# Performance work log

Measured on AMD Instinct MI355X. Metric: run time of the kernel, lower is better.

Reference implementation:

```python
import jax, jax.numpy as jnp
import numpy as np

B, S, D = 1, 2048, 2048
H = 16
Q_LORA = 1536
KV_LORA = 512
NOPE = 128
ROPE = 64
VD = 128
QHD = NOPE + ROPE  # 192
THETA = 50000.0
EPS = 1e-6


def rmsnorm(x, w, eps=EPS):
    xf = x.astype(jnp.float32)
    var = jnp.mean(xf * xf, axis=-1, keepdims=True)
    return (w * (xf * jax.lax.rsqrt(var + eps)).astype(x.dtype))


def rotate_half(x):
    x1, x2 = jnp.split(x, 2, axis=-1)
    return jnp.concatenate([-x2, x1], axis=-1)


def deinterleave(x):
    # view(..., d//2, 2).transpose(-1,-2).reshape(..., d): [x0,x2,...,x1,x3,...]
    b, h, s, d = x.shape
    return x.reshape(b, h, s, d // 2, 2).swapaxes(-1, -2).reshape(b, h, s, d)


def setup_inputs() -> dict:
    key = jax.random.key(0)
    ks = jax.random.split(key, 8)
    sc = 0.02
    return {
        "hidden_states": jax.random.normal(ks[0], (B, S, D), jnp.float32),
        "position_ids": jnp.broadcast_to(jnp.arange(S, dtype=jnp.int32), (B, S)),
        "q_a_w": jax.random.normal(ks[1], (Q_LORA, D), jnp.float32) * sc,
        "q_a_ln_w": jnp.ones((Q_LORA,), jnp.float32),
        "q_b_w": jax.random.normal(ks[2], (H * QHD, Q_LORA), jnp.float32) * sc,
        "kv_a_w": jax.random.normal(ks[3], (KV_LORA + ROPE, D), jnp.float32) * sc,
        "kv_a_ln_w": jnp.ones((KV_LORA,), jnp.float32),
        "kv_b_w": jax.random.normal(ks[4], (H * (NOPE + VD), KV_LORA), jnp.float32) * sc,
        "o_w": jax.random.normal(ks[5], (D, H * VD), jnp.float32) * sc,
    }


def reference(hidden_states, position_ids, q_a_w, q_a_ln_w, q_b_w, kv_a_w, kv_a_ln_w, kv_b_w, o_w):
    bsz, q_len, _ = hidden_states.shape
    # low-rank Q: q_b(rmsnorm(q_a(x)))
    q = rmsnorm(hidden_states @ q_a_w.T, q_a_ln_w) @ q_b_w.T
    q = q.reshape(bsz, q_len, H, QHD).transpose(0, 2, 1, 3)  # [b,h,s,192]
    q_nope, q_pe = q[..., :NOPE], q[..., NOPE:]
    # compressed KV + shared rope key
    ckv = hidden_states @ kv_a_w.T  # [b,s,512+64]
    compressed_kv, k_pe = ckv[..., :KV_LORA], ckv[..., KV_LORA:]
    k_pe = k_pe.reshape(bsz, q_len, 1, ROPE).transpose(0, 2, 1, 3)  # [b,1,s,64]
    kv = rmsnorm(compressed_kv, kv_a_ln_w) @ kv_b_w.T
    kv = kv.reshape(bsz, q_len, H, NOPE + VD).transpose(0, 2, 1, 3)
    k_nope, value_states = kv[..., :NOPE], kv[..., NOPE:]
    # rotary cache
    inv_freq = 1.0 / (THETA ** (jnp.arange(0, ROPE, 2, dtype=jnp.float32) / ROPE))
    t = jnp.arange(q_len, dtype=jnp.float32)
    freqs = jnp.outer(t, inv_freq)
    emb = jnp.concatenate([freqs, freqs], axis=-1)  # [s,64]
    cos = jnp.cos(emb)[position_ids][:, None]  # [b,1,s,64]
    sin = jnp.sin(emb)[position_ids][:, None]
    q_pe = deinterleave(q_pe)
    k_pe = deinterleave(k_pe)
    q_pe = q_pe * cos + rotate_half(q_pe) * sin
    k_pe = k_pe * cos + rotate_half(k_pe) * sin
    query_states = jnp.concatenate([q_nope, q_pe], axis=-1)  # [b,h,s,192]
    key_states = jnp.concatenate([k_nope, jnp.broadcast_to(k_pe, (bsz, H, q_len, ROPE))], axis=-1)
    scale = QHD ** (-0.5)
    scores = jnp.einsum('bhqd,bhkd->bhqk', query_states, key_states) * scale
    causal = jnp.tril(jnp.ones((q_len, q_len), bool))
    scores = jnp.where(causal, scores, jnp.finfo(scores.dtype).min)
    attn = jax.nn.softmax(scores, axis=-1)
    out = jnp.einsum('bhqk,bhkd->bhqd', attn, value_states)  # [b,h,s,128]
    out = out.transpose(0, 2, 1, 3).reshape(bsz, q_len, H * VD)
    return out @ o_w.T
```

## Files before the change

### kernel.cpp

```cpp
#include <hip/hip_runtime.h>
#include <hip/hip_bf16.h>
#include <cmath>

#define S_LEN 2048
#define D_MODEL 2048
#define N_HEADS 16
#define Q_LORA 1536
#define KV_LORA 512
#define NOPE 128
#define ROPE_D 64
#define VD 128
#define QHD 192
#define AC_W 2112

typedef __attribute__((ext_vector_type(8))) short bf16x8;
typedef __attribute__((ext_vector_type(4))) float f32x4;
typedef __attribute__((ext_vector_type(4))) unsigned short u16x4;

static __device__ __forceinline__ unsigned short f2u(float x) {
  union { float f; unsigned u; } v; v.f = x;
  unsigned r = v.u + 0x7fffu + ((v.u >> 16) & 1u);
  return (unsigned short)(r >> 16);
}
static __device__ __forceinline__ unsigned short f2u_fast(float x) {
  union { float f; unsigned u; } v; v.f = x;
  return (unsigned short)((v.u + 0x8000u) >> 16);
}
static __device__ __forceinline__ float u2f(unsigned short x) {
  union { unsigned u; float f; } v; v.u = ((unsigned)x) << 16;
  return v.f;
}

#define AS1 __attribute__((address_space(1)))
#define AS3 __attribute__((address_space(3)))
static __device__ __forceinline__ void gload_lds16(const unsigned short* g, unsigned short* l) {
  __builtin_amdgcn_global_load_lds((const AS1 unsigned int*)g, (AS3 unsigned int*)l, 16, 0, 0);
}

__global__ __launch_bounds__(256) void conv_bf16(const float* __restrict__ src,
                                                 unsigned short* __restrict__ dst,
                                                 int n4, float scale) {
  for (int i = blockIdx.x * 256 + threadIdx.x; i < n4; i += gridDim.x * 256) {
    const float4 v = ((const float4*)src)[i];
    u16x4 o;
    o[0] = f2u(v.x * scale); o[1] = f2u(v.y * scale);
    o[2] = f2u(v.z * scale); o[3] = f2u(v.w * scale);
    ((u16x4*)dst)[i] = o;
  }
}

__global__ __launch_bounds__(256) void conv2_bf16(const float* __restrict__ srcA, int n4a,
                                                  const float* __restrict__ srcB, int n4total,
                                                  unsigned short* __restrict__ dst) {
  for (int i = blockIdx.x * 256 + threadIdx.x; i < n4total; i += gridDim.x * 256) {
    const float4 v = (i < n4a) ? ((const float4*)srcA)[i] : ((const float4*)srcB)[i - n4a];
    u16x4 o;
    o[0] = f2u(v.x); o[1] = f2u(v.y); o[2] = f2u(v.z); o[3] = f2u(v.w);
    ((u16x4*)dst)[i] = o;
  }
}

template <int MODE>
__global__ __launch_bounds__(256) void gemm_mfma(const unsigned short* __restrict__ A,
                                                 const unsigned short* __restrict__ W,
                                                 void* __restrict__ Cv,
                                                 unsigned short* __restrict__ C2,
                                                 int N, int K) {
  __shared__ unsigned short As[2][8192];
  __shared__ unsigned short Ws[2][4096];
  const int tid = threadIdx.x;
  const int wave = tid >> 6, lane = tid & 63;
  const int col16 = lane & 15, g = lane >> 4;
  const int arow = blockIdx.y * 128, wrow = blockIdx.x * 64;
  const int wm = (wave >> 1) * 64, wn = (wave & 1) * 32;

  const unsigned short* gA[4];
  const unsigned short* gW[2];
  int dA[4], dW[2];
#pragma unroll
  for (int i = 0; i < 4; ++i) {
    const int c = i * 256 + tid;
    const int r = c >> 3, sl = c & 7;
    gA[i] = A + (size_t)(arow + r) * K + (sl ^ (r & 7)) * 8;
    dA[i] = c * 8;
  }
#pragma unroll
  for (int i = 0; i < 2; ++i) {
    const int c = i * 256 + tid;
    const int r = c >> 3, sl = c & 7;
    gW[i] = W + (size_t)(wrow + r) * K + (sl ^ (r & 7)) * 8;
    dW[i] = c * 8;
  }

  f32x4 acc[4][2];
#pragma unroll
  for (int i = 0; i < 4; ++i)
#pragma unroll
    for (int j = 0; j < 2; ++j) acc[i][j] = (f32x4){0.f, 0.f, 0.f, 0.f};

#pragma unroll
  for (int i = 0; i < 4; ++i) gload_lds16(gA[i], &As[0][dA[i]]);
#pragma unroll
  for (int i = 0; i < 2; ++i) gload_lds16(gW[i], &Ws[0][dW[i]]);

  int cur = 0;
  for (int k0 = 0; k0 < K; k0 += 64) {
    __syncthreads();
    if (k0 + 64 < K) {
      const int b = cur ^ 1, kk = k0 + 64;
#pragma unroll
      for (int i = 0; i < 4; ++i) gload_lds16(gA[i] + kk, &As[b][dA[i]]);
#pragma unroll
      for (int i = 0; i < 2; ++i) gload_lds16(gW[i] + kk, &Ws[b][dW[i]]);
    }
#pragma unroll
    for (int kh = 0; kh < 2; ++kh) {
      bf16x8 af[4], bfr[2];
#pragma unroll
      for (int i = 0; i < 4; ++i) {
        const int row = wm + i * 16 + col16;
        af[i] = *(const bf16x8*)(&As[cur][row * 64 + (((kh * 4 + g) ^ (row & 7)) * 8)]);
      }
#pragma unroll
      for (int j = 0; j < 2; ++j) {
        const int row = wn + j * 16 + col16;
        bfr[j] = *(const bf16x8*)(&Ws[cur][row * 64 + (((kh * 4 + g) ^ (row & 7)) * 8)]);
      }
#pragma unroll
      for (int i = 0; i < 4; ++i)
#pragma unroll
        for (int j = 0; j < 2; ++j)
          acc[i][j] = __builtin_amdgcn_mfma_f32_16x16x32_bf16(af[i], bfr[j], acc[i][j], 0, 0, 0);
    }
    cur ^= 1;
  }

#pragma unroll
  for (int i = 0; i < 4; ++i)
#pragma unroll
    for (int j = 0; j < 2; ++j) {
      const int col = wrow + wn + j * 16 + col16;
      const int row0 = arow + wm + i * 16 + g * 4;
#pragma unroll
      for (int r = 0; r < 4; ++r) {
        if constexpr (MODE == 0)
          ((float*)Cv)[(size_t)(row0 + r) * N + col] = acc[i][j][r];
        else if constexpr (MODE == 1)
          ((unsigned short*)Cv)[(size_t)(row0 + r) * N + col] = f2u(acc[i][j][r]);
        else {
          const int hh = col >> 8, d = col & 255;
          if (d < NOPE)
            C2[((size_t)hh * S_LEN + row0 + r) * QHD + d] = f2u(acc[i][j][r]);
          else
            ((unsigned short*)Cv)[(size_t)(row0 + r) * (N_HEADS * 256) + col] = f2u(acc[i][j][r]);
        }
      }
    }
}

__global__ __launch_bounds__(256) void rmsnorm2_kernel(const float* __restrict__ ac,
                                                       const float* __restrict__ wq,
                                                       const float* __restrict__ wkv,
                                                       unsigned short* __restrict__ qan,
                                                       unsigned short* __restrict__ ckvn) {
  const int row = blockIdx.x;
  const bool kv = blockIdx.y != 0;
  const float* x = ac + (size_t)row * AC_W + (kv ? Q_LORA : 0);
  const float* w = kv ? wkv : wq;
  unsigned short* dst = kv ? (ckvn + (size_t)row * KV_LORA) : (qan + (size_t)row * Q_LORA);
  const int dim = kv ? KV_LORA : Q_LORA;
  float ss = 0.f;
  for (int i = threadIdx.x; i < dim; i += 256) {
    float v = x[i];
    ss += v * v;
  }
#pragma unroll
  for (int off = 32; off; off >>= 1) ss += __shfl_xor(ss, off);
  __shared__ float red[4];
  const int wv = threadIdx.x >> 6, ln = threadIdx.x & 63;
  if (ln == 0) red[wv] = ss;
  __syncthreads();
  const float tot = red[0] + red[1] + red[2] + red[3];
  const float scale = rsqrtf(tot / (float)dim + 1e-6f);
  for (int i = threadIdx.x; i < dim; i += 256) {
    dst[i] = f2u(w[i] * (x[i] * scale));
  }
}

__global__ void rope_kernel(unsigned short* __restrict__ q, const float* __restrict__ ac,
                            unsigned short* __restrict__ Kb, const int* __restrict__ pos_ids) {
  const int s = blockIdx.x;
  const int j = threadIdx.x;
  const float t = (float)pos_ids[s];
  const float invf = powf(50000.0f, -(float)(2 * j) / 64.0f);
  const float ang = t * invf;
  const float c = cosf(ang), sn = sinf(ang);
  for (int h = 0; h < N_HEADS; ++h) {
    unsigned short* base = q + (size_t)s * (N_HEADS * QHD) + h * QHD + NOPE;
    const float x0 = u2f(base[2 * j]), x1 = u2f(base[2 * j + 1]);
    __syncthreads();
    base[j] = f2u(x0 * c - x1 * sn);
    base[32 + j] = f2u(x1 * c + x0 * sn);
    __syncthreads();
  }
  const float* kb = ac + (size_t)s * AC_W + 2048;
  const unsigned short r0 = f2u(kb[2 * j] * c - kb[2 * j + 1] * sn);
  const unsigned short r1 = f2u(kb[2 * j + 1] * c + kb[2 * j] * sn);
#pragma unroll
  for (int h = 0; h < N_HEADS; ++h) {
    unsigned short* kd = Kb + ((size_t)h * S_LEN + s) * QHD + NOPE;
    kd[j] = r0;
    kd[32 + j] = r1;
  }
}

__global__ __launch_bounds__(256) void build_vt(const unsigned short* __restrict__ kv,
                                                unsigned short* __restrict__ Vt) {
  __shared__ unsigned short t[32][33];
  const int s0 = blockIdx.x * 32, d0 = blockIdx.y * 32, h = blockIdx.z;
  const int tx = threadIdx.x & 31, ty = threadIdx.x >> 5;
#pragma unroll
  for (int i = 0; i < 4; ++i) {
    const int s = s0 + ty + i * 8;
    t[ty + i * 8][tx] = kv[(size_t)s * (N_HEADS * 256) + h * 256 + NOPE + d0 + tx];
  }
  __syncthreads();
  const int p = ((tx & 15) >> 2) * 8 + ((tx >> 4) & 1) * 4 + (tx & 3);
#pragma unroll
  for (int i = 0; i < 4; ++i) {
    const int d = d0 + ty + i * 8;
    Vt[((size_t)h * VD + d) * S_LEN + s0 + p] = t[tx][ty + i * 8];
  }
}

__global__ __launch_bounds__(256, 4) void flash_attn(const unsigned short* __restrict__ Q,
                                                     const unsigned short* __restrict__ Kb,
                                                     const unsigned short* __restrict__ Vt,
                                                     unsigned short* __restrict__ Pb,
                                                     float2* __restrict__ mlb) {
  __shared__ unsigned short Ks[2][32 * QHD];
  __shared__ unsigned short Vs[2][VD * 32];
  const int tid = threadIdx.x;
  const int wave = tid >> 6, lane = tid & 63;
  const int g = lane >> 4, col = lane & 15;
  const int lin = (int)blockIdx.x;
  const int h = ((lin & 7) << 1) | ((lin >> 3) & 1);
  const int s = (lin >> 4) & 1;
  const int z = lin >> 5;
  int t;
  if (z < 8) t = 31 - z;
  else if (z < 16) t = z - 8;
  else if (z < 24) t = 39 - z;
  else t = z - 16;
  const int qw = t * 64 + wave * 16;
  const int qr = qw + col;

  bf16x8 qf[6];
  {
    const unsigned short* qrow = Q + (size_t)qr * (N_HEADS * QHD) + h * QHD + g * 8;
#pragma unroll
    for (int i = 0; i < 6; ++i) qf[i] = *(const bf16x8*)(qrow + i * 32);
  }

  const unsigned short* KbH = Kb + (size_t)h * S_LEN * QHD;
  const unsigned short* VtH = Vt + (size_t)h * VD * S_LEN;

  int eK[3], eV[2];
#pragma unroll
  for (int i = 0; i < 3; ++i) {
    const int c = i * 256 + tid;
    const int r = c / 24, sl = c - r * 24;
    eK[i] = r * QHD + (((sl & 24) | ((sl & 7) ^ (r & 7)))) * 8;
  }
#pragma unroll
  for (int i = 0; i < 2; ++i) {
    const int c = i * 256 + tid;
    const int d = c >> 2, sl = c & 3;
    eV[i] = d * S_LEN + ((sl ^ (d & 3))) * 8;
  }

  f32x4 o[8];
#pragma unroll
  for (int i = 0; i < 8; ++i) o[i] = (f32x4){0.f, 0.f, 0.f, 0.f};
  float m = -1e30f, l = 0.f;

  const int nT = t + 1;

  {
    const unsigned short* kp = KbH + (size_t)s * 32 * QHD;
    const unsigned short* vp = VtH + s * 32;
#pragma unroll
    for (int i = 0; i < 3; ++i) gload_lds16(kp + eK[i], &Ks[0][(i * 256 + tid) * 8]);
#pragma unroll
    for (int i = 0; i < 2; ++i) gload_lds16(vp + eV[i], &Vs[0][(i * 256 + tid) * 8]);
  }

  int xK[6];
#pragma unroll
  for (int i = 0; i < 6; ++i) xK[i] = ((4 * i + g) ^ (col & 7)) * 8;
  const int rbK = col * QHD;
  const int xV = (g ^ (col & 3)) * 8;
  const int rbV = col * 32;

  for (int it = 0; it < nT; ++it) {
    __syncthreads();
    if (it + 1 < nT) {
      const int jn = 2 * (it + 1) + s;
      const unsigned short* kp = KbH + (size_t)jn * 32 * QHD;
      const unsigned short* vp = VtH + jn * 32;
      const int b = (it + 1) & 1;
#pragma unroll
      for (int i = 0; i < 3; ++i) gload_lds16(kp + eK[i], &Ks[b][(i * 256 + tid) * 8]);
#pragma unroll
      for (int i = 0; i < 2; ++i) gload_lds16(vp + eV[i], &Vs[b][(i * 256 + tid) * 8]);
    }
    const int k0 = 32 * (2 * it + s);
    if (k0 <= qw + 15) {
      const unsigned short* Ksc = Ks[it & 1];
      const unsigned short* Vsc = Vs[it & 1];

      f32x4 c0 = (f32x4){0.f, 0.f, 0.f, 0.f}, c1 = (f32x4){0.f, 0.f, 0.f, 0.f};
      __builtin_amdgcn_s_setprio(1);
#pragma unroll
      for (int dt = 0; dt < 6; ++dt) {
        const bf16x8 a0 = *(const bf16x8*)(Ksc + rbK + xK[dt]);
        const bf16x8 a1 = *(const bf16x8*)(Ksc + rbK + 16 * QHD + xK[dt]);
        c0 = __builtin_amdgcn_mfma_f32_16x16x32_bf16(a0, qf[dt], c0, 0, 0, 0);
        c1 = __builtin_amdgcn_mfma_f32_16x16x32_bf16(a1, qf[dt], c1, 0, 0, 0);
      }
      __builtin_amdgcn_s_setprio(0);

      if (k0 + 31 > qw) {
#pragma unroll
        for (int r = 0; r < 4; ++r) {
          const int kk = k0 + 4 * g + r;
          if (kk > qr) c0[r] = -1e30f;
          if (kk + 16 > qr) c1[r] = -1e30f;
        }
      }
      float bm = fmaxf(fmaxf(fmaxf(c0[0], c0[1]), fmaxf(c0[2], c0[3])),
                       fmaxf(fmaxf(c1[0], c1[1]), fmaxf(c1[2], c1[3])));
      bm = fmaxf(bm, __shfl_xor(bm, 16));
      bm = fmaxf(bm, __shfl_xor(bm, 32));
      const bool skip = __all(bm <= m + 8.f);
      const float mn = skip ? m : fmaxf(m, bm);
      float ps = 0.f;
      bf16x8 pb;
#pragma unroll
      for (int r = 0; r < 4; ++r) {
        const float p0 = exp2f(c0[r] - mn);
        const float p1 = exp2f(c1[r] - mn);
        ps += p0 + p1;
        pb[r] = (short)f2u_fast(p0);
        pb[4 + r] = (short)f2u_fast(p1);
      }
      ps += __shfl_xor(ps, 16);
      ps += __shfl_xor(ps, 32);
      if (skip) {
        l += ps;
      } else {
        const float corr = exp2f(m - mn);
        l = l * corr + ps;
        m = mn;
#pragma unroll
        for (int i = 0; i < 8; ++i) {
          o[i][0] *= corr; o[i][1] *= corr; o[i][2] *= corr; o[i][3] *= corr;
        }
      }
      __builtin_amdgcn_s_setprio(1);
#pragma unroll
      for (int db = 0; db < 8; ++db) {
        const bf16x8 va = *(const bf16x8*)(Vsc + db * 512 + rbV + xV);
        o[db] = __builtin_amdgcn_mfma_f32_16x16x32_bf16(va, pb, o[db], 0, 0, 0);
      }
      __builtin_amdgcn_s_setprio(0);
    }
  }

  unsigned short* pr = Pb + (((size_t)qr * 2 + s) * N_HEADS + h) * VD;
#pragma unroll
  for (int db = 0; db < 8; ++db) {
    u16x4 w4;
#pragma unroll
    for (int r = 0; r < 4; ++r) w4[r] = f2u(o[db][r]);
    *(uint2*)(pr + db * 16 + 4 * g) = __builtin_bit_cast(uint2, w4);
  }
  if (g == 0) mlb[((size_t)qr * 2 + s) * N_HEADS + h] = make_float2(m, l);
}

__global__ __launch_bounds__(256) void combine2(const unsigned short* __restrict__ Pb,
                                                const float2* __restrict__ mlb,
                                                unsigned short* __restrict__ outb) {
  const int idx = blockIdx.x * 256 + threadIdx.x;
  const int d8 = idx & 15, hq = idx >> 4;
  const int h = hq & 15, q = hq >> 4;
  const float2 a = mlb[((size_t)q * 2 + 0) * N_HEADS + h];
  const float2 b = mlb[((size_t)q * 2 + 1) * N_HEADS + h];
  const float M = fmaxf(a.x, b.x);
  float wA = exp2f(a.x - M), wB = exp2f(b.x - M);
  const float inv = 1.f / (wA * a.y + wB * b.y);
  wA *= inv; wB *= inv;
  const bf16x8 v0 = *(const bf16x8*)(Pb + (((size_t)q * 2 + 0) * N_HEADS + h) * VD + d8 * 8);
  const bf16x8 v1 = *(const bf16x8*)(Pb + (((size_t)q * 2 + 1) * N_HEADS + h) * VD + d8 * 8);
  u16x4 o0, o1;
#pragma unroll
  for (int e = 0; e < 4; ++e) {
    o0[e] = f2u(u2f((unsigned short)v0[e]) * wA + u2f((unsigned short)v1[e]) * wB);
    o1[e] = f2u(u2f((unsigned short)v0[4 + e]) * wA + u2f((unsigned short)v1[4 + e]) * wB);
  }
  unsigned short* dst = outb + ((size_t)q * N_HEADS + h) * VD + d8 * 8;
  *(uint2*)(dst) = __builtin_bit_cast(uint2, o0);
  *(uint2*)(dst + 4) = __builtin_bit_cast(uint2, o1);
}

extern "C" void kernel_launch(void* const* d_in, const int* in_sizes, int n_in,
                              void* d_out, int out_size, void* d_ws, size_t ws_size,
                              hipStream_t stream) {
  const float* hidden    = (const float*)d_in[0];
  const int*   pos       = (const int*)d_in[1];
  const float* q_a_w     = (const float*)d_in[2];
  const float* q_a_ln_w  = (const float*)d_in[3];
  const float* q_b_w     = (const float*)d_in[4];
  const float* kv_a_w    = (const float*)d_in[5];
  const float* kv_a_ln_w = (const float*)d_in[6];
  const float* kv_b_w    = (const float*)d_in[7];
  const float* o_w       = (const float*)d_in[8];
  float* out = (float*)d_out;
  (void)in_sizes; (void)n_in; (void)out_size; (void)ws_size;

  char* base = (char*)d_ws;
  unsigned short* qbuf  = (unsigned short*)(base);
  unsigned short* kvbuf = (unsigned short*)(base + 12582912);
  unsigned short* Pbuf  = (unsigned short*)(base + 12582912);
  float*          ac    = (float*)(base + 29360128);
  unsigned short* qan   = (unsigned short*)(base + 46661632);
  float2*         mlb   = (float2*)(base + 46661632);
  unsigned short* ckvn  = (unsigned short*)(base + 52953088);
  unsigned short* Hb    = (unsigned short*)(base + 55050240);
  unsigned short* Vt    = (unsigned short*)(base + 55050240);
  unsigned short* wbuf  = (unsigned short*)(base + 63438848);
  unsigned short* attnb = (unsigned short*)(base + 72876032);
  unsigned short* Kb    = (unsigned short*)(base + 81264640);

  const dim3 b256(256);
  const float qscale = 0.07216878364870323f * 1.4426950408889634f;

  conv_bf16<<<2048, b256, 0, stream>>>(hidden, Hb, (S_LEN * D_MODEL) / 4, 1.f);

  conv2_bf16<<<2048, b256, 0, stream>>>(q_a_w, (Q_LORA * D_MODEL) / 4,
                                        kv_a_w, (AC_W * D_MODEL) / 4, wbuf);
  gemm_mfma<0><<<dim3(AC_W / 64, S_LEN / 128), b256, 0, stream>>>(Hb, wbuf, ac, nullptr, AC_W, D_MODEL);

  rmsnorm2_kernel<<<dim3(S_LEN, 2), b256, 0, stream>>>(ac, q_a_ln_w, kv_a_ln_w, qan, ckvn);

  conv_bf16<<<2048, b256, 0, stream>>>(q_b_w, wbuf, (N_HEADS * QHD * Q_LORA) / 4, qscale);
  gemm_mfma<1><<<dim3(N_HEADS * QHD / 64, S_LEN / 128), b256, 0, stream>>>(qan, wbuf, qbuf, nullptr, N_HEADS * QHD, Q_LORA);

  conv_bf16<<<2048, b256, 0, stream>>>(kv_b_w, wbuf, (N_HEADS * 256 * KV_LORA) / 4, 1.f);
  gemm_mfma<2><<<dim3(N_HEADS * 256 / 64, S_LEN / 128), b256, 0, stream>>>(ckvn, wbuf, kvbuf, Kb, N_HEADS * 256, KV_LORA);

  rope_kernel<<<S_LEN, 32, 0, stream>>>(qbuf, ac, Kb, pos);

  build_vt<<<dim3(S_LEN / 32, VD / 32, N_HEADS), b256, 0, stream>>>(kvbuf, Vt);

  flash_attn<<<dim3(1024), b256, 0, stream>>>(qbuf, Kb, Vt, Pbuf, mlb);
  combine2<<<2048, b256, 0, stream>>>(Pbuf, mlb, attnb);

  conv_bf16<<<2048, b256, 0, stream>>>(o_w, wbuf, (D_MODEL * N_HEADS * VD) / 4, 1.f);
  gemm_mfma<0><<<dim3(D_MODEL / 64, S_LEN / 128), b256, 0, stream>>>(attnb, wbuf, out, nullptr, D_MODEL, N_HEADS * VD);
}
```

Baseline: 204.7 us.

## Fuse weight conversion kernels and write V transposed directly from kv_b GEMM

```diff
diff --git a/kernel.cpp b/kernel.cpp
--- a/kernel.cpp
+++ b/kernel.cpp
@@ -49,14 +49,51 @@
   }
 }
 
-__global__ __launch_bounds__(256) void conv2_bf16(const float* __restrict__ srcA, int n4a,
-                                                  const float* __restrict__ srcB, int n4total,
-                                                  unsigned short* __restrict__ dst) {
-  for (int i = blockIdx.x * 256 + threadIdx.x; i < n4total; i += gridDim.x * 256) {
-    const float4 v = (i < n4a) ? ((const float4*)srcA)[i] : ((const float4*)srcB)[i - n4a];
-    u16x4 o;
-    o[0] = f2u(v.x); o[1] = f2u(v.y); o[2] = f2u(v.z); o[3] = f2u(v.w);
-    ((u16x4*)dst)[i] = o;
+__global__ __launch_bounds__(256) void conv_stage1(const float* __restrict__ hidden,
+                                                   const float* __restrict__ qaw,
+                                                   const float* __restrict__ kvaw,
+                                                   unsigned short* __restrict__ Hb,
+                                                   unsigned short* __restrict__ wbuf) {
+  const int nH = (S_LEN * D_MODEL) / 4;
+  const int nQ = (Q_LORA * D_MODEL) / 4;
+  const int nT = nH + nQ + ((KV_LORA + ROPE_D) * D_MODEL) / 4;
+  for (int i = blockIdx.x * 256 + threadIdx.x; i < nT; i += gridDim.x * 256) {
+    float4 v;
+    unsigned short* dst;
+    int o;
+    if (i < nH) {
+      v = ((const float4*)hidden)[i]; dst = Hb; o = i;
+    } else {
+      o = i - nH;
+      v = (o < nQ) ? ((const float4*)qaw)[o] : ((const float4*)kvaw)[o - nQ];
+      dst = wbuf;
+    }
+    u16x4 u;
+    u[0] = f2u(v.x); u[1] = f2u(v.y); u[2] = f2u(v.z); u[3] = f2u(v.w);
+    ((u16x4*)dst)[o] = u;
+  }
+}
+
+__global__ __launch_bounds__(256) void conv_stage2(const float* __restrict__ qbw,
+                                                   const float* __restrict__ kvbsrc,
+                                                   unsigned short* __restrict__ wbuf,
+                                                   unsigned short* __restrict__ kvbw,
+                                                   float qscale) {
+  const int nQB = (N_HEADS * QHD * Q_LORA) / 4;
+  const int nT = nQB + (N_HEADS * 256 * KV_LORA) / 4;
+  for (int i = blockIdx.x * 256 + threadIdx.x; i < nT; i += gridDim.x * 256) {
+    u16x4 u;
+    if (i < nQB) {
+      const float4 v = ((const float4*)qbw)[i];
+      u[0] = f2u(v.x * qscale); u[1] = f2u(v.y * qscale);
+      u[2] = f2u(v.z * qscale); u[3] = f2u(v.w * qscale);
+      ((u16x4*)wbuf)[i] = u;
+    } else {
+      const int o = i - nQB;
+      const float4 v = ((const float4*)kvbsrc)[o];
+      u[0] = f2u(v.x); u[1] = f2u(v.y); u[2] = f2u(v.z); u[3] = f2u(v.w);
+      ((u16x4*)kvbw)[o] = u;
+    }
   }
 }
 
@@ -141,18 +178,28 @@
     for (int j = 0; j < 2; ++j) {
       const int col = wrow + wn + j * 16 + col16;
       const int row0 = arow + wm + i * 16 + g * 4;
-#pragma unroll
-      for (int r = 0; r < 4; ++r) {
-        if constexpr (MODE == 0)
+      if constexpr (MODE == 0) {
+#pragma unroll
+        for (int r = 0; r < 4; ++r)
           ((float*)Cv)[(size_t)(row0 + r) * N + col] = acc[i][j][r];
-        else if constexpr (MODE == 1)
+      } else if constexpr (MODE == 1) {
+#pragma unroll
+        for (int r = 0; r < 4; ++r)
           ((unsigned short*)Cv)[(size_t)(row0 + r) * N + col] = f2u(acc[i][j][r]);
-        else {
-          const int hh = col >> 8, d = col & 255;
-          if (d < NOPE)
+      } else {
+        const int hh = col >> 8, d = col & 255;
+        if (d < NOPE) {
+#pragma unroll
+          for (int r = 0; r < 4; ++r)
             C2[((size_t)hh * S_LEN + row0 + r) * QHD + d] = f2u(acc[i][j][r]);
-          else
-            ((unsigned short*)Cv)[(size_t)(row0 + r) * (N_HEADS * 256) + col] = f2u(acc[i][j][r]);
+        } else {
+          const int dv = d - NOPE;
+          const int p0 = ((row0 & 15) >> 2) * 8 + ((row0 >> 4) & 1) * 4;
+          u16x4 w4;
+#pragma unroll
+          for (int r = 0; r < 4; ++r) w4[r] = f2u(acc[i][j][r]);
+          *(uint2*)((unsigned short*)Cv + ((size_t)hh * VD + dv) * S_LEN + (row0 & ~31) + p0) =
+              __builtin_bit_cast(uint2, w4);
         }
       }
     }
@@ -211,25 +258,6 @@
     unsigned short* kd = Kb + ((size_t)h * S_LEN + s) * QHD + NOPE;
     kd[j] = r0;
     kd[32 + j] = r1;
-  }
-}
-
-__global__ __launch_bounds__(256) void build_vt(const unsigned short* __restrict__ kv,
-                                                unsigned short* __restrict__ Vt) {
-  __shared__ unsigned short t[32][33];
-  const int s0 = blockIdx.x * 32, d0 = blockIdx.y * 32, h = blockIdx.z;
-  const int tx = threadIdx.x & 31, ty = threadIdx.x >> 5;
-#pragma unroll
-  for (int i = 0; i < 4; ++i) {
-    const int s = s0 + ty + i * 8;
-    t[ty + i * 8][tx] = kv[(size_t)s * (N_HEADS * 256) + h * 256 + NOPE + d0 + tx];
-  }
-  __syncthreads();
-  const int p = ((tx & 15) >> 2) * 8 + ((tx >> 4) & 1) * 4 + (tx & 3);
-#pragma unroll
-  for (int i = 0; i < 4; ++i) {
-    const int d = d0 + ty + i * 8;
-    Vt[((size_t)h * VD + d) * S_LEN + s0 + p] = t[tx][ty + i * 8];
   }
 }
 
@@ -430,7 +458,6 @@
 
   char* base = (char*)d_ws;
   unsigned short* qbuf  = (unsigned short*)(base);
-  unsigned short* kvbuf = (unsigned short*)(base + 12582912);
   unsigned short* Pbuf  = (unsigned short*)(base + 12582912);
   float*          ac    = (float*)(base + 29360128);
   unsigned short* qan   = (unsigned short*)(base + 46661632);
@@ -440,28 +467,25 @@
   unsigned short* Vt    = (unsigned short*)(base + 55050240);
   unsigned short* wbuf  = (unsigned short*)(base + 63438848);
   unsigned short* attnb = (unsigned short*)(base + 72876032);
+  unsigned short* kvbw  = (unsigned short*)(base + 72876032);
   unsigned short* Kb    = (unsigned short*)(base + 81264640);
 
   const dim3 b256(256);
   const float qscale = 0.07216878364870323f * 1.4426950408889634f;
 
-  conv_bf16<<<2048, b256, 0, stream>>>(hidden, Hb, (S_LEN * D_MODEL) / 4, 1.f);
-
-  conv2_bf16<<<2048, b256, 0, stream>>>(q_a_w, (Q_LORA * D_MODEL) / 4,
-                                        kv_a_w, (AC_W * D_MODEL) / 4, wbuf);
+  conv_stage1<<<2048, b256, 0, stream>>>(hidden, q_a_w, kv_a_w, Hb, wbuf);
+
   gemm_mfma<0><<<dim3(AC_W / 64, S_LEN / 128), b256, 0, stream>>>(Hb, wbuf, ac, nullptr, AC_W, D_MODEL);
 
   rmsnorm2_kernel<<<dim3(S_LEN, 2), b256, 0, stream>>>(ac, q_a_ln_w, kv_a_ln_w, qan, ckvn);
 
-  conv_bf16<<<2048, b256, 0, stream>>>(q_b_w, wbuf, (N_HEADS * QHD * Q_LORA) / 4, qscale);
+  conv_stage2<<<2048, b256, 0, stream>>>(q_b_w, kv_b_w, wbuf, kvbw, qscale);
+
   gemm_mfma<1><<<dim3(N_HEADS * QHD / 64, S_LEN / 128), b256, 0, stream>>>(qan, wbuf, qbuf, nullptr, N_HEADS * QHD, Q_LORA);
 
-  conv_bf16<<<2048, b256, 0, stream>>>(kv_b_w, wbuf, (N_HEADS * 256 * KV_LORA) / 4, 1.f);
-  gemm_mfma<2><<<dim3(N_HEADS * 256 / 64, S_LEN / 128), b256, 0, stream>>>(ckvn, wbuf, kvbuf, Kb, N_HEADS * 256, KV_LORA);
+  gemm_mfma<2><<<dim3(N_HEADS * 256 / 64, S_LEN / 128), b256, 0, stream>>>(ckvn, kvbw, Vt, Kb, N_HEADS * 256, KV_LORA);
 
   rope_kernel<<<S_LEN, 32, 0, stream>>>(qbuf, ac, Kb, pos);
-
-  build_vt<<<dim3(S_LEN / 32, VD / 32, N_HEADS), b256, 0, stream>>>(kvbuf, Vt);
 
   flash_attn<<<dim3(1024), b256, 0, stream>>>(qbuf, Kb, Vt, Pbuf, mlb);
   combine2<<<2048, b256, 0, stream>>>(Pbuf, mlb, attnb);
```

New measurement: 195.9 us. 1.04x faster.
